# Performance work log

Hardware: AMD Instinct MI355X
Metric: run time of the kernel (lower is better)

The kernel has to match this reference:

```python
import itertools
import jax, jax.numpy as jnp
import numpy as np

TAU = 1e-06


def build_A_system(M: int) -> np.ndarray:
    """All binary matrices A in {0,1}^{2 x M} with exactly one 1 per column,
    excluding the two assignments where one group is empty. Shape [K, 2, M],
    K = 2^M - 2."""
    mats = []
    for assign in itertools.product([0, 1], repeat=M):
        s = sum(assign)
        if s == 0 or s == M:
            continue
        A = np.zeros((2, M), dtype=np.float32)
        for i, val in enumerate(assign):
            A[val, i] = 1.0
        mats.append(A)
    return np.stack(mats, axis=0)


def setup_inputs() -> dict:
    key = jax.random.key(0)
    k1, k2 = jax.random.split(key)
    B, M, T = 8, 8, 32000
    estimated_sources = jax.random.normal(k1, (B, M, T), dtype=jnp.float32)
    input_mixtures = jax.random.normal(k2, (B, 2, T), dtype=jnp.float32)
    return {"estimated_sources": estimated_sources, "input_mixtures": input_mixtures}


def reference(estimated_sources, input_mixtures):
    B, M, T = estimated_sources.shape
    assert input_mixtures.shape[1] == 2
    # [K, 2, M] binary assignment matrices (static, built at trace time)
    A = jnp.asarray(build_A_system(M), dtype=estimated_sources.dtype)
    # Remix estimated sources under every assignment: [B, K, 2, T]
    est = jnp.einsum('kjm,bmt->bkjt', A, estimated_sources)
    # Per-mixture input energy: [B, 2]
    input_energy = jnp.sum(input_mixtures ** 2, axis=-1)
    # Noise energy per (batch, combo, mixture): [B, K, 2]
    noise_energy = jnp.sum((input_mixtures[:, None, :, :] - est) ** 2, axis=-1)
    ie = input_energy[:, None, :]  # [B, 1, 2] broadcast over K
    # Negative SNR in dB: [B, K, 2]
    snr_loss = -10.0 * jnp.log10(ie / (noise_energy + TAU * ie))
    # Sum over the two mixtures, minimize over assignments, mean over batch
    per_combo = jnp.sum(snr_loss, axis=-1)     # [B, K]
    per_sample = jnp.min(per_combo, axis=-1)   # [B]
    return jnp.mean(per_sample)
```

## Files before the change

kernel.cpp:

```cpp
#include <hip/hip_runtime.h>
#include <math.h>

#define TAU 1e-6f

constexpr int Mm = 8;
constexpr int Bb = 8;
constexpr int Tt = 32000;
constexpr int NCOL = Tt / 4;
constexpr int BLKS_PER_B = 16;
constexpr int NSTAT = 54;
constexpr int WS_STRIDE = 64;

#define STAT_LIST(X) \
  X(e0,0) X(e1,1) \
  X(c00,2) X(c01,3) X(c02,4) X(c03,5) X(c04,6) X(c05,7) X(c06,8) X(c07,9) \
  X(c10,10) X(c11,11) X(c12,12) X(c13,13) X(c14,14) X(c15,15) X(c16,16) X(c17,17) \
  X(g00,18) X(g01,19) X(g02,20) X(g03,21) X(g04,22) X(g05,23) X(g06,24) X(g07,25) \
  X(g11,26) X(g12,27) X(g13,28) X(g14,29) X(g15,30) X(g16,31) X(g17,32) \
  X(g22,33) X(g23,34) X(g24,35) X(g25,36) X(g26,37) X(g27,38) \
  X(g33,39) X(g34,40) X(g35,41) X(g36,42) X(g37,43) \
  X(g44,44) X(g45,45) X(g46,46) X(g47,47) \
  X(g55,48) X(g56,49) X(g57,50) \
  X(g66,51) X(g67,52) \
  X(g77,53)

#define DECL_STAT(v,i) float v = 0.0f;

#define COMP_UPDATE(F) do { \
  const float x0 = x0v.F, x1 = x1v.F; \
  const float t0 = s0v.F, t1 = s1v.F, t2 = s2v.F, t3 = s3v.F; \
  const float t4 = s4v.F, t5 = s5v.F, t6 = s6v.F, t7 = s7v.F; \
  e0 = fmaf(x0, x0, e0);  e1 = fmaf(x1, x1, e1); \
  c00 = fmaf(x0, t0, c00); c01 = fmaf(x0, t1, c01); c02 = fmaf(x0, t2, c02); c03 = fmaf(x0, t3, c03); \
  c04 = fmaf(x0, t4, c04); c05 = fmaf(x0, t5, c05); c06 = fmaf(x0, t6, c06); c07 = fmaf(x0, t7, c07); \
  c10 = fmaf(x1, t0, c10); c11 = fmaf(x1, t1, c11); c12 = fmaf(x1, t2, c12); c13 = fmaf(x1, t3, c13); \
  c14 = fmaf(x1, t4, c14); c15 = fmaf(x1, t5, c15); c16 = fmaf(x1, t6, c16); c17 = fmaf(x1, t7, c17); \
  g00 = fmaf(t0, t0, g00); g01 = fmaf(t0, t1, g01); g02 = fmaf(t0, t2, g02); g03 = fmaf(t0, t3, g03); \
  g04 = fmaf(t0, t4, g04); g05 = fmaf(t0, t5, g05); g06 = fmaf(t0, t6, g06); g07 = fmaf(t0, t7, g07); \
  g11 = fmaf(t1, t1, g11); g12 = fmaf(t1, t2, g12); g13 = fmaf(t1, t3, g13); g14 = fmaf(t1, t4, g14); \
  g15 = fmaf(t1, t5, g15); g16 = fmaf(t1, t6, g16); g17 = fmaf(t1, t7, g17); \
  g22 = fmaf(t2, t2, g22); g23 = fmaf(t2, t3, g23); g24 = fmaf(t2, t4, g24); g25 = fmaf(t2, t5, g25); \
  g26 = fmaf(t2, t6, g26); g27 = fmaf(t2, t7, g27); \
  g33 = fmaf(t3, t3, g33); g34 = fmaf(t3, t4, g34); g35 = fmaf(t3, t5, g35); g36 = fmaf(t3, t6, g36); \
  g37 = fmaf(t3, t7, g37); \
  g44 = fmaf(t4, t4, g44); g45 = fmaf(t4, t5, g45); g46 = fmaf(t4, t6, g46); g47 = fmaf(t4, t7, g47); \
  g55 = fmaf(t5, t5, g55); g56 = fmaf(t5, t6, g56); g57 = fmaf(t5, t7, g57); \
  g66 = fmaf(t6, t6, g66); g67 = fmaf(t6, t7, g67); \
  g77 = fmaf(t7, t7, g77); \
} while (0)

#define REDUCE_STORE(v,i) { \
  float r_ = v; \
  r_ += __shfl_down(r_, 32, 64); r_ += __shfl_down(r_, 16, 64); \
  r_ += __shfl_down(r_, 8, 64);  r_ += __shfl_down(r_, 4, 64); \
  r_ += __shfl_down(r_, 2, 64);  r_ += __shfl_down(r_, 1, 64); \
  if (lane == 0) sh[wv][i] = r_; \
}

__global__ void __launch_bounds__(256) mixit_reduce_kernel(
    const float* __restrict__ es,
    const float* __restrict__ im,
    float* __restrict__ ws) {
    const int b   = blockIdx.y;
    const int tid = threadIdx.x;

    STAT_LIST(DECL_STAT)

    const float4* esb4 = (const float4*)(es + (size_t)b * Mm * Tt);
    const float4* imb4 = (const float4*)(im + (size_t)b * 2 * Tt);

    for (int col = blockIdx.x * blockDim.x + tid; col < NCOL;
         col += BLKS_PER_B * blockDim.x) {
        const float4 x0v = imb4[col];
        const float4 x1v = imb4[NCOL + col];
        const float4 s0v = esb4[0 * NCOL + col];
        const float4 s1v = esb4[1 * NCOL + col];
        const float4 s2v = esb4[2 * NCOL + col];
        const float4 s3v = esb4[3 * NCOL + col];
        const float4 s4v = esb4[4 * NCOL + col];
        const float4 s5v = esb4[5 * NCOL + col];
        const float4 s6v = esb4[6 * NCOL + col];
        const float4 s7v = esb4[7 * NCOL + col];
        COMP_UPDATE(x);
        COMP_UPDATE(y);
        COMP_UPDATE(z);
        COMP_UPDATE(w);
    }

    __shared__ float sh[4][NSTAT];
    const int lane = tid & 63;
    const int wv   = tid >> 6;

    STAT_LIST(REDUCE_STORE)

    __syncthreads();
    if (tid < NSTAT) {
        const float p = sh[0][tid] + sh[1][tid] + sh[2][tid] + sh[3][tid];
        ws[((size_t)b * BLKS_PER_B + blockIdx.x) * WS_STRIDE + tid] = p;
    }
}

__global__ void __launch_bounds__(512) mixit_finalize_kernel(
    const float* __restrict__ ws,
    float* __restrict__ out) {
    __shared__ float stats[Bb][NSTAT];
    __shared__ float minb[Bb];
    const int tid = threadIdx.x;

    for (int i = tid; i < Bb * NSTAT; i += 512) {
        const int b = i / NSTAT, s = i % NSTAT;
        const float* base = ws + (size_t)b * BLKS_PER_B * WS_STRIDE + s;
        float acc = 0.0f;
#pragma unroll
        for (int k = 0; k < BLKS_PER_B; ++k) acc += base[k * WS_STRIDE];
        stats[b][s] = acc;
    }
    __syncthreads();

    const int wv   = tid >> 6;
    const int lane = tid & 63;
    const float* st = stats[wv];
    const float E0 = st[0];
    const float E1 = st[1];

    float vmin = INFINITY;
#pragma unroll
    for (int ci = 0; ci < 4; ++ci) {
        const int cm1 = lane + 64 * ci;
        if (cm1 < 254) {
            const int c = cm1 + 1;
            float ne0 = E0;
            float ne1 = E1;
#pragma unroll
            for (int m = 0; m < Mm; ++m) {
                if ((c >> m) & 1) ne1 -= 2.0f * st[10 + m];
                else              ne0 -= 2.0f * st[2 + m];
            }
            int p = 18;
#pragma unroll
            for (int m = 0; m < Mm; ++m) {
#pragma unroll
                for (int mp = m; mp < Mm; ++mp, ++p) {
                    const float g = st[p];
                    const float w = (m == mp) ? 1.0f : 2.0f;
                    const int bm  = (c >> m) & 1;
                    const int bmp = (c >> mp) & 1;
                    if (bm & bmp)         ne1 += w * g;
                    else if (!(bm | bmp)) ne0 += w * g;
                }
            }
            const float snr = 10.0f * log10f((ne0 + TAU * E0) / E0)
                            + 10.0f * log10f((ne1 + TAU * E1) / E1);
            vmin = fminf(vmin, snr);
        }
    }
#pragma unroll
    for (int off = 32; off > 0; off >>= 1) vmin = fminf(vmin, __shfl_down(vmin, off, 64));
    if (lane == 0) minb[wv] = vmin;
    __syncthreads();

    if (tid == 0) {
        float tot = 0.0f;
#pragma unroll
        for (int i = 0; i < Bb; ++i) tot += minb[i];
        out[0] = tot / (float)Bb;
    }
}

extern "C" void kernel_launch(void* const* d_in, const int* in_sizes, int n_in,
                              void* d_out, int out_size, void* d_ws, size_t ws_size,
                              hipStream_t stream) {
    const float* es = (const float*)d_in[0];
    const float* im = (const float*)d_in[1];
    float* out = (float*)d_out;
    float* ws  = (float*)d_ws;

    dim3 grid(BLKS_PER_B, Bb);
    mixit_reduce_kernel<<<grid, 256, 0, stream>>>(es, im, ws);
    mixit_finalize_kernel<<<1, 512, 0, stream>>>(ws, out);
}
```

Measured before the change: 28.07 us.

## Fuse reduce and finalize kernels via cooperative launch and grid sync

Merges the partial-statistics reduction and the finalize step into one cooperative kernel. A grid-wide sync separates them, and block 0 then does the finalize work, with each wave handling two batches instead of one. This removes the second kernel launch and its gap. In exchange it adds a grid barrier and the overhead of a cooperative launch, and the finalize now runs with half as many threads.

After: 68.31 us. +143.3%, slower.

```diff
diff --git a/kernel.cpp b/kernel.cpp
--- a/kernel.cpp
+++ b/kernel.cpp
@@ -1,5 +1,8 @@
 #include <hip/hip_runtime.h>
+#include <hip/hip_cooperative_groups.h>
 #include <math.h>
+
+namespace cg = cooperative_groups;
 
 #define TAU 1e-6f
 
@@ -8,6 +11,7 @@
 constexpr int Tt = 32000;
 constexpr int NCOL = Tt / 4;
 constexpr int BLKS_PER_B = 16;
+constexpr int NBLK = BLKS_PER_B * Bb;
 constexpr int NSTAT = 54;
 constexpr int WS_STRIDE = 64;
 
@@ -57,20 +61,21 @@
   if (lane == 0) sh[wv][i] = r_; \
 }
 
-__global__ void __launch_bounds__(256) mixit_reduce_kernel(
+__global__ void __launch_bounds__(256) mixit_fused_kernel(
     const float* __restrict__ es,
     const float* __restrict__ im,
-    float* __restrict__ ws) {
-    const int b   = blockIdx.y;
+    float* __restrict__ ws,
+    float* __restrict__ out) {
     const int tid = threadIdx.x;
+    const int b   = blockIdx.x >> 4;
+    const int blk = blockIdx.x & 15;
 
     STAT_LIST(DECL_STAT)
 
     const float4* esb4 = (const float4*)(es + (size_t)b * Mm * Tt);
     const float4* imb4 = (const float4*)(im + (size_t)b * 2 * Tt);
 
-    for (int col = blockIdx.x * blockDim.x + tid; col < NCOL;
-         col += BLKS_PER_B * blockDim.x) {
+    for (int col = blk * 256 + tid; col < NCOL; col += BLKS_PER_B * 256) {
         const float4 x0v = imb4[col];
         const float4 x1v = imb4[NCOL + col];
         const float4 s0v = esb4[0 * NCOL + col];
@@ -87,76 +92,84 @@
         COMP_UPDATE(w);
     }
 
-    __shared__ float sh[4][NSTAT];
-    const int lane = tid & 63;
-    const int wv   = tid >> 6;
+    {
+        __shared__ float sh[4][NSTAT];
+        const int lane = tid & 63;
+        const int wv   = tid >> 6;
 
-    STAT_LIST(REDUCE_STORE)
+        STAT_LIST(REDUCE_STORE)
 
-    __syncthreads();
-    if (tid < NSTAT) {
-        const float p = sh[0][tid] + sh[1][tid] + sh[2][tid] + sh[3][tid];
-        ws[((size_t)b * BLKS_PER_B + blockIdx.x) * WS_STRIDE + tid] = p;
+        __syncthreads();
+        if (tid < NSTAT) {
+            const float p = sh[0][tid] + sh[1][tid] + sh[2][tid] + sh[3][tid];
+            ws[(size_t)blockIdx.x * WS_STRIDE + tid] = p;
+        }
     }
-}
 
-__global__ void __launch_bounds__(512) mixit_finalize_kernel(
-    const float* __restrict__ ws,
-    float* __restrict__ out) {
+    __threadfence();
+    cg::this_grid().sync();
+    if (blockIdx.x != 0) return;
+    __threadfence();
+
     __shared__ float stats[Bb][NSTAT];
     __shared__ float minb[Bb];
-    const int tid = threadIdx.x;
 
-    for (int i = tid; i < Bb * NSTAT; i += 512) {
-        const int b = i / NSTAT, s = i % NSTAT;
-        const float* base = ws + (size_t)b * BLKS_PER_B * WS_STRIDE + s;
+    for (int i = tid; i < Bb * NSTAT; i += 256) {
+        const int bb = i / NSTAT, s = i % NSTAT;
+        const float* base = ws + (size_t)bb * BLKS_PER_B * WS_STRIDE + s;
         float acc = 0.0f;
 #pragma unroll
         for (int k = 0; k < BLKS_PER_B; ++k) acc += base[k * WS_STRIDE];
-        stats[b][s] = acc;
+        stats[bb][s] = acc;
     }
     __syncthreads();
 
     const int wv   = tid >> 6;
     const int lane = tid & 63;
-    const float* st = stats[wv];
-    const float E0 = st[0];
-    const float E1 = st[1];
 
-    float vmin = INFINITY;
 #pragma unroll
-    for (int ci = 0; ci < 4; ++ci) {
-        const int cm1 = lane + 64 * ci;
-        if (cm1 < 254) {
-            const int c = cm1 + 1;
-            float ne0 = E0;
-            float ne1 = E1;
+    for (int rep = 0; rep < 2; ++rep) {
+        const int bb = wv + 4 * rep;
+        const float* st = stats[bb];
+        const float E0 = st[0];
+        const float E1 = st[1];
+
+        float vmin = INFINITY;
 #pragma unroll
-            for (int m = 0; m < Mm; ++m) {
-                if ((c >> m) & 1) ne1 -= 2.0f * st[10 + m];
-                else              ne0 -= 2.0f * st[2 + m];
+        for (int ci = 0; ci < 4; ++ci) {
+            const int cm1 = lane + 64 * ci;
+            if (cm1 < 254) {
+                const int c = cm1 + 1;
+                float ne0 = E0;
+                float ne1 = E1;
+#pragma unroll
+                for (int m = 0; m < Mm; ++m) {
+                    if ((c >> m) & 1) ne1 -= 2.0f * st[10 + m];
+                    else              ne0 -= 2.0f * st[2 + m];
+                }
+                int p = 18;
+#pragma unroll
+                for (int m = 0; m < Mm; ++m) {
+#pragma unroll
+                    for (int mp = m; mp < Mm; ++mp, ++p) {
+                        const float g = st[p];
+                        const float w = (m == mp) ? 1.0f : 2.0f;
+                        const int bm  = (c >> m) & 1;
+                        const int bmp = (c >> mp) & 1;
+                        if (bm & bmp)         ne1 += w * g;
+                        else if (!(bm | bmp)) ne0 += w * g;
+                    }
+                }
+                const float snr = 10.0f * log10f((ne0 + TAU * E0) / E0)
+                                + 10.0f * log10f((ne1 + TAU * E1) / E1);
+                vmin = fminf(vmin, snr);
             }
-            int p = 18;
+        }
 #pragma unroll
-            for (int m = 0; m < Mm; ++m) {
-#pragma unroll
-                for (int mp = m; mp < Mm; ++mp, ++p) {
-                    const float g = st[p];
-                    const float w = (m == mp) ? 1.0f : 2.0f;
-                    const int bm  = (c >> m) & 1;
-                    const int bmp = (c >> mp) & 1;
-                    if (bm & bmp)         ne1 += w * g;
-                    else if (!(bm | bmp)) ne0 += w * g;
-                }
-            }
-            const float snr = 10.0f * log10f((ne0 + TAU * E0) / E0)
-                            + 10.0f * log10f((ne1 + TAU * E1) / E1);
-            vmin = fminf(vmin, snr);
-        }
+        for (int off = 32; off > 0; off >>= 1)
+            vmin = fminf(vmin, __shfl_down(vmin, off, 64));
+        if (lane == 0) minb[bb] = vmin;
     }
-#pragma unroll
-    for (int off = 32; off > 0; off >>= 1) vmin = fminf(vmin, __shfl_down(vmin, off, 64));
-    if (lane == 0) minb[wv] = vmin;
     __syncthreads();
 
     if (tid == 0) {
@@ -175,7 +188,7 @@
     float* out = (float*)d_out;
     float* ws  = (float*)d_ws;
 
-    dim3 grid(BLKS_PER_B, Bb);
-    mixit_reduce_kernel<<<grid, 256, 0, stream>>>(es, im, ws);
-    mixit_finalize_kernel<<<1, 512, 0, stream>>>(ws, out);
+    void* args[] = { (void*)&es, (void*)&im, (void*)&ws, (void*)&out };
+    hipLaunchCooperativeKernel((void*)mixit_fused_kernel,
+                               dim3(NBLK), dim3(256), args, 0, stream);
 }
```

## Use one column per thread across 256 blocks and minimize SNR via product

Applied to the files above, without the earlier changes.

The reduce kernel now launches 32 blocks per batch on a flat grid, so each thread handles exactly one float4 column instead of looping. This spreads the memory-bound reduction over more CUs. The finalize kernel compares the product of the two noise energies per assignment and takes a single log10 after the min, since the sum of the two logs is monotone in that product. The per-combination transcendental work is removed, and finalize reads twice as many partial rows.

Measured after the change: 29.34 us, median of 2. +4.5%, slower.

```diff
diff --git a/kernel.cpp b/kernel.cpp
--- a/kernel.cpp
+++ b/kernel.cpp
@@ -7,7 +7,8 @@
 constexpr int Bb = 8;
 constexpr int Tt = 32000;
 constexpr int NCOL = Tt / 4;
-constexpr int BLKS_PER_B = 16;
+constexpr int BLKS_PER_B = 32;
+constexpr int NBLK = BLKS_PER_B * Bb;
 constexpr int NSTAT = 54;
 constexpr int WS_STRIDE = 64;
 
@@ -57,20 +58,20 @@
   if (lane == 0) sh[wv][i] = r_; \
 }
 
-__global__ void __launch_bounds__(256) mixit_reduce_kernel(
+__global__ void __launch_bounds__(256, 1) mixit_reduce_kernel(
     const float* __restrict__ es,
     const float* __restrict__ im,
     float* __restrict__ ws) {
-    const int b   = blockIdx.y;
     const int tid = threadIdx.x;
+    const int b   = blockIdx.x >> 5;
+    const int blk = blockIdx.x & 31;
+    const int col = blk * 256 + tid;
 
     STAT_LIST(DECL_STAT)
 
-    const float4* esb4 = (const float4*)(es + (size_t)b * Mm * Tt);
-    const float4* imb4 = (const float4*)(im + (size_t)b * 2 * Tt);
-
-    for (int col = blockIdx.x * blockDim.x + tid; col < NCOL;
-         col += BLKS_PER_B * blockDim.x) {
+    if (col < NCOL) {
+        const float4* esb4 = (const float4*)(es + (size_t)b * Mm * Tt);
+        const float4* imb4 = (const float4*)(im + (size_t)b * 2 * Tt);
         const float4 x0v = imb4[col];
         const float4 x1v = imb4[NCOL + col];
         const float4 s0v = esb4[0 * NCOL + col];
@@ -88,15 +89,15 @@
     }
 
     __shared__ float sh[4][NSTAT];
-    const int lane = tid & 63;
-    const int wv   = tid >> 6;
-
-    STAT_LIST(REDUCE_STORE)
-
+    {
+        const int lane = tid & 63;
+        const int wv   = tid >> 6;
+        STAT_LIST(REDUCE_STORE)
+    }
     __syncthreads();
     if (tid < NSTAT) {
-        const float p = sh[0][tid] + sh[1][tid] + sh[2][tid] + sh[3][tid];
-        ws[((size_t)b * BLKS_PER_B + blockIdx.x) * WS_STRIDE + tid] = p;
+        ws[(size_t)blockIdx.x * WS_STRIDE + tid] =
+            sh[0][tid] + sh[1][tid] + sh[2][tid] + sh[3][tid];
     }
 }
 
@@ -107,13 +108,13 @@
     __shared__ float minb[Bb];
     const int tid = threadIdx.x;
 
-    for (int i = tid; i < Bb * NSTAT; i += 512) {
-        const int b = i / NSTAT, s = i % NSTAT;
-        const float* base = ws + (size_t)b * BLKS_PER_B * WS_STRIDE + s;
+    if (tid < Bb * NSTAT) {
+        const int bb = tid / NSTAT, s = tid - bb * NSTAT;
+        const float* base = ws + (size_t)bb * BLKS_PER_B * WS_STRIDE + s;
         float acc = 0.0f;
 #pragma unroll
         for (int k = 0; k < BLKS_PER_B; ++k) acc += base[k * WS_STRIDE];
-        stats[b][s] = acc;
+        stats[bb][s] = acc;
     }
     __syncthreads();
 
@@ -123,10 +124,10 @@
     const float E0 = st[0];
     const float E1 = st[1];
 
-    float vmin = INFINITY;
-#pragma unroll
+    float qmin = INFINITY;
+#pragma unroll 1
     for (int ci = 0; ci < 4; ++ci) {
-        const int cm1 = lane + 64 * ci;
+        const int cm1 = lane + (ci << 6);
         if (cm1 < 254) {
             const int c = cm1 + 1;
             float ne0 = E0;
@@ -149,14 +150,13 @@
                     else if (!(bm | bmp)) ne0 += w * g;
                 }
             }
-            const float snr = 10.0f * log10f((ne0 + TAU * E0) / E0)
-                            + 10.0f * log10f((ne1 + TAU * E1) / E1);
-            vmin = fminf(vmin, snr);
+            qmin = fminf(qmin, (ne0 + TAU * E0) * (ne1 + TAU * E1));
         }
     }
 #pragma unroll
-    for (int off = 32; off > 0; off >>= 1) vmin = fminf(vmin, __shfl_down(vmin, off, 64));
-    if (lane == 0) minb[wv] = vmin;
+    for (int off = 32; off > 0; off >>= 1)
+        qmin = fminf(qmin, __shfl_down(qmin, off, 64));
+    if (lane == 0) minb[wv] = 10.0f * log10f(qmin / (E0 * E1));
     __syncthreads();
 
     if (tid == 0) {
@@ -175,7 +175,6 @@
     float* out = (float*)d_out;
     float* ws  = (float*)d_ws;
 
-    dim3 grid(BLKS_PER_B, Bb);
-    mixit_reduce_kernel<<<grid, 256, 0, stream>>>(es, im, ws);
+    mixit_reduce_kernel<<<dim3(NBLK), dim3(256), 0, stream>>>(es, im, ws);
     mixit_finalize_kernel<<<1, 512, 0, stream>>>(ws, out);
 }
```
